# Optimization experiments

Measured on AMD Instinct MI355X. Metric: run time of the kernel, lower is better.

Reference implementation:

```python
import jax, jax.numpy as jnp
import numpy as np

NUM_GRAPHS = 2048
BN_EPS = 1e-5


def gcn_conv(x, W, b, src, dst, deg_isqrt):
    # PyG GCNConv: out = D^{-1/2} (A + I) D^{-1/2} X W + b
    h = x @ W  # [N, H]
    norm = deg_isqrt[src] * deg_isqrt[dst]  # [E]
    msg = h[src] * norm[:, None]            # [E, H]
    agg = jax.ops.segment_sum(msg, dst, num_segments=x.shape[0])
    agg = agg + h * (deg_isqrt * deg_isqrt)[:, None]  # self-loop term
    return agg + b


def batch_norm(x, gamma, beta):
    # training-mode BatchNorm1d over nodes (biased variance)
    mean = jnp.mean(x, axis=0)
    var = jnp.mean(jnp.square(x - mean), axis=0)
    return gamma * (x - mean) * jax.lax.rsqrt(var + BN_EPS) + beta


def pools(x, batch):
    ones = jnp.ones((x.shape[0],), x.dtype)
    cnt = jax.ops.segment_sum(ones, batch, num_segments=NUM_GRAPHS)  # [G]
    mean_p = jax.ops.segment_sum(x, batch, num_segments=NUM_GRAPHS) / jnp.maximum(cnt, 1.0)[:, None]
    max_p = jax.ops.segment_max(x, batch, num_segments=NUM_GRAPHS)
    max_p = jnp.where(cnt[:, None] > 0, max_p, 0.0)
    return jnp.concatenate([mean_p, max_p], axis=1)  # [G, 2H]


def setup_inputs() -> dict:
    key = jax.random.key(0)
    ks = jax.random.split(key, 32)
    N, E, D, H = 100000, 300000, 8, 256
    x = jax.random.normal(ks[0], (N, D), jnp.float32)
    edge_index = jax.random.randint(ks[1], (2, E), 0, N, jnp.int64)
    batch = jnp.sort(jax.random.randint(ks[2], (N,), 0, NUM_GRAPHS, jnp.int64))

    def lin(k, fi, fo):
        s = 1.0 / np.sqrt(fi)
        kw, kb = jax.random.split(k)
        return (jax.random.uniform(kw, (fi, fo), jnp.float32, -s, s),
                jax.random.uniform(kb, (fo,), jnp.float32, -s, s))

    W1, b1 = lin(ks[3], D, H)
    W2, b2 = lin(ks[4], H, H)
    W3, b3 = lin(ks[5], H, H)
    W4, b4 = lin(ks[6], H, H)
    g = jnp.ones((H,), jnp.float32)
    be = jnp.zeros((H,), jnp.float32)
    sW1, sb1 = lin(ks[7], 2 * H, 256)
    sW2, sb2 = lin(ks[8], 256, 128)
    hW1 = jnp.stack([lin(ks[9 + i], 128, 32)[0] for i in range(3)])
    hb1 = jnp.stack([lin(ks[9 + i], 128, 32)[1] for i in range(3)])
    hW2 = jnp.stack([lin(ks[12 + i], 32, 1)[0] for i in range(3)])
    hb2 = jnp.stack([lin(ks[12 + i], 32, 1)[1] for i in range(3)])
    return dict(x=x, edge_index=edge_index, batch=batch,
                W1=W1, b1=b1, W2=W2, b2=b2, W3=W3, b3=b3, W4=W4, b4=b4,
                g1=g, be1=be, g2=g, be2=be, g3=g, be3=be, g4=g, be4=be,
                sW1=sW1, sb1=sb1, sW2=sW2, sb2=sb2,
                hW1=hW1, hb1=hb1, hW2=hW2, hb2=hb2)


def reference(x, edge_index, batch, W1, b1, W2, b2, W3, b3, W4, b4,
              g1, be1, g2, be2, g3, be3, g4, be4,
              sW1, sb1, sW2, sb2, hW1, hb1, hW2, hb2):
    src, dst = edge_index[0], edge_index[1]
    N = x.shape[0]
    # degree with self-loops (GCN normalization)
    deg = jax.ops.segment_sum(jnp.ones((src.shape[0],), x.dtype), dst, num_segments=N) + 1.0
    deg_isqrt = jax.lax.rsqrt(deg)

    h = jax.nn.relu(batch_norm(gcn_conv(x, W1, b1, src, dst, deg_isqrt), g1, be1))
    h = jax.nn.relu(batch_norm(gcn_conv(h, W2, b2, src, dst, deg_isqrt), g2, be2))
    h = jax.nn.relu(batch_norm(gcn_conv(h, W3, b3, src, dst, deg_isqrt), g3, be3))
    h = jax.nn.relu(batch_norm(gcn_conv(h, W4, b4, src, dst, deg_isqrt), g4, be4))

    pooled = pools(h, batch)                               # [G, 512]
    s = jax.nn.relu(pooled @ sW1 + sb1)                    # dropout: eval -> identity
    s = jax.nn.relu(s @ sW2 + sb2)                         # [G, 128]
    # heads (vectorized over 3 tasks): [T, G]
    t = jax.nn.relu(jnp.einsum('gf,tfo->tgo', s, hW1) + hb1[:, None, :])
    out = (jnp.einsum('tgo,tof->tgf', t, hW2) + hb2[:, None, :])[..., 0]
    return out  # [num_tasks, G] == stacked list of squeezed head outputs
```

## Files before the change

### kernel.cpp

```cpp
#include <hip/hip_runtime.h>
#include <math.h>

#define TPB 256
#define NGRAPH 2048

typedef __attribute__((ext_vector_type(8))) short bf16x8;
typedef __attribute__((ext_vector_type(4))) float f32x4;

__device__ __forceinline__ unsigned short f2bf(float f) {
  unsigned u = __float_as_uint(f);
  unsigned r = (u + 0x7FFF + ((u >> 16) & 1)) >> 16;
  return (unsigned short)r;
}
__device__ __forceinline__ float bf2f(unsigned short h) {
  return __uint_as_float(((unsigned)h) << 16);
}

#define GLOAD_LDS16(G, L) \
  __builtin_amdgcn_global_load_lds((const __attribute__((address_space(1))) unsigned int*)(G), \
                                   (__attribute__((address_space(3))) unsigned int*)(L), 16, 0, 0)

__global__ void k_init(float* __restrict__ deg, int* __restrict__ cnt,
                       int* __restrict__ cntg, float* __restrict__ statsAll,
                       float* __restrict__ statsP, int N) {
  int i = blockIdx.x * TPB + threadIdx.x;
  if (i < N) { deg[i] = 1.0f; cnt[i] = 0; }
  if (i < NGRAPH) cntg[i] = 0;
  if (i < 2048) statsAll[i] = 0.f;
  if (i < 12288) statsP[i] = 0.f;
}

__global__ void k_deg_hist(const int* __restrict__ dst, float* __restrict__ deg,
                           int* __restrict__ cnt, int E) {
  int e = blockIdx.x * TPB + threadIdx.x;
  if (e < E) {
    int d = dst[e];
    atomicAdd(&deg[d], 1.0f);
    atomicAdd(&cnt[d], 1);
  }
}

__global__ void k_hist_batch(const int* __restrict__ batch, int* __restrict__ cntg, int N) {
  int i = blockIdx.x * TPB + threadIdx.x;
  if (i < N) atomicAdd(&cntg[batch[i]], 1);
}

__global__ void k_rsqrt(float* __restrict__ d, int N) {
  int i = blockIdx.x * TPB + threadIdx.x;
  if (i < N) d[i] = rsqrtf(d[i]);
}

__global__ void k_scan1(const int* __restrict__ in, int* __restrict__ out,
                        int* __restrict__ bsum, int n) {
  __shared__ int ts[256];
  int tid = threadIdx.x;
  int base = blockIdx.x * 1024 + tid * 4;
  int v0 = (base + 0 < n) ? in[base + 0] : 0;
  int v1 = (base + 1 < n) ? in[base + 1] : 0;
  int v2 = (base + 2 < n) ? in[base + 2] : 0;
  int v3 = (base + 3 < n) ? in[base + 3] : 0;
  int s = v0 + v1 + v2 + v3;
  int run = s;
  ts[tid] = run; __syncthreads();
  for (int off = 1; off < 256; off <<= 1) {
    int add = (tid >= off) ? ts[tid - off] : 0;
    __syncthreads();
    run += add; ts[tid] = run; __syncthreads();
  }
  int acc = run - s;
  if (base + 0 < n) out[base + 0] = acc; acc += v0;
  if (base + 1 < n) out[base + 1] = acc; acc += v1;
  if (base + 2 < n) out[base + 2] = acc; acc += v2;
  if (base + 3 < n) out[base + 3] = acc;
  if (tid == 255) bsum[blockIdx.x] = run;
}

__global__ void k_scan_small(const int* __restrict__ in, int* __restrict__ dst, int n) {
  __shared__ int ts[256];
  int tid = threadIdx.x;
  int chunk = (n + 255) >> 8;
  int start = tid * chunk;
  int s = 0;
  for (int j = 0; j < chunk; ++j) { int idx = start + j; if (idx < n) s += in[idx]; }
  int run = s;
  ts[tid] = run; __syncthreads();
  for (int off = 1; off < 256; off <<= 1) {
    int add = (tid >= off) ? ts[tid - off] : 0;
    __syncthreads();
    run += add; ts[tid] = run; __syncthreads();
  }
  int acc = run - s;
  for (int j = 0; j < chunk; ++j) {
    int idx = start + j;
    if (idx < n) { dst[idx] = acc; acc += in[idx]; }
  }
  if (tid == 255) dst[n] = run;
}

__global__ void k_scan3(int* __restrict__ rs, const int* __restrict__ bsumx,
                        int* __restrict__ cursor, int n, int total) {
  int i = blockIdx.x * TPB + threadIdx.x;
  if (i < n) {
    int v = rs[i] + bsumx[i >> 10];
    rs[i] = v; cursor[i] = v;
  }
  if (i == 0) rs[n] = total;
}

__global__ void k_scatter(const int* __restrict__ src, const int* __restrict__ dst,
                          int* __restrict__ cursor, int* __restrict__ es, int E) {
  int e = blockIdx.x * TPB + threadIdx.x;
  if (e < E) {
    int d = dst[e];
    int p = atomicAdd(&cursor[d], 1);
    es[p] = src[e];
  }
}

__global__ __launch_bounds__(256) void k_wprep2(const float* __restrict__ W,
    unsigned short* __restrict__ Wblk) {
  int c = blockIdx.x, k = threadIdx.x;
  float w = W[k * 256 + c];
  int t = k >> 6, kl = k & 63;
  Wblk[t * 16384 + c * 64 + (kl ^ ((c & 7) << 3))] = f2bf(w);
}

__global__ void k_agg8(const float* __restrict__ x, const float* __restrict__ dis,
                       const int* __restrict__ rs, const int* __restrict__ es,
                       float* __restrict__ xa8, int N) {
  int t = blockIdx.x * TPB + threadIdx.x;
  int n = t >> 3, c = t & 7;
  if (n >= N) return;
  int e0 = rs[n], e1 = rs[n + 1];
  float acc = 0.f;
  for (int e = e0; e < e1; ++e) {
    int s = es[e];
    acc += dis[s] * x[s * 8 + c];
  }
  float dn = dis[n];
  xa8[n * 8 + c] = dn * acc + dn * dn * x[n * 8 + c];
}

__global__ __launch_bounds__(256) void k_gemm8(const float* __restrict__ A,
    const float* __restrict__ W, const float* __restrict__ b,
    unsigned short* __restrict__ Ybf, float* __restrict__ stats, int N) {
  __shared__ float Ws[8 * 256];
  __shared__ float bs[256];
  __shared__ float rows[64 * 8];
  int tid = threadIdx.x;
  int row0 = blockIdx.x * 64;
  for (int j = 0; j < 8; ++j) Ws[tid + j * 256] = W[tid + j * 256];
  bs[tid] = b[tid];
  int lim = N * 8;
  int o0 = row0 * 8 + tid, o1 = o0 + 256;
  rows[tid] = (o0 < lim) ? A[o0] : 0.f;
  rows[tid + 256] = (o1 < lim) ? A[o1] : 0.f;
  __syncthreads();
  float s = 0.f, s2 = 0.f;
  for (int r = 0; r < 64; ++r) {
    int row = row0 + r;
    if (row >= N) break;
    float acc = bs[tid];
#pragma unroll
    for (int k = 0; k < 8; ++k) acc += rows[r * 8 + k] * Ws[k * 256 + tid];
    Ybf[(size_t)row * 256 + tid] = f2bf(acc);
    s += acc; s2 += acc * acc;
  }
  atomicAdd(&stats[tid], s);
  atomicAdd(&stats[256 + tid], s2);
}

__global__ __launch_bounds__(256) void k_agg_bn(const unsigned short* __restrict__ Ybf,
    const float* __restrict__ ss, const float* __restrict__ dis,
    const int* __restrict__ rs, const int* __restrict__ es,
    unsigned short* __restrict__ Ahi, int N) {
  int lane = threadIdx.x & 63;
  int n = __builtin_amdgcn_readfirstlane(blockIdx.x * 4 + (threadIdx.x >> 6));
  if (n >= N) return;
  int c = lane * 4;
  float4 sc = *(const float4*)&ss[c];
  float4 sh = *(const float4*)&ss[256 + c];
  int e0 = rs[n], e1 = rs[n + 1];
  float4 a = make_float4(0.f, 0.f, 0.f, 0.f);
  int e = e0;
  for (; e + 2 <= e1; e += 2) {
    int s0 = es[e], s1 = es[e + 1];
    float d0 = dis[s0], d1 = dis[s1];
    ushort4 y0 = *(const ushort4*)&Ybf[(size_t)s0 * 256 + c];
    ushort4 y1 = *(const ushort4*)&Ybf[(size_t)s1 * 256 + c];
    a.x += d0 * fmaxf(fmaf(bf2f(y0.x), sc.x, sh.x), 0.f)
         + d1 * fmaxf(fmaf(bf2f(y1.x), sc.x, sh.x), 0.f);
    a.y += d0 * fmaxf(fmaf(bf2f(y0.y), sc.y, sh.y), 0.f)
         + d1 * fmaxf(fmaf(bf2f(y1.y), sc.y, sh.y), 0.f);
    a.z += d0 * fmaxf(fmaf(bf2f(y0.z), sc.z, sh.z), 0.f)
         + d1 * fmaxf(fmaf(bf2f(y1.z), sc.z, sh.z), 0.f);
    a.w += d0 * fmaxf(fmaf(bf2f(y0.w), sc.w, sh.w), 0.f)
         + d1 * fmaxf(fmaf(bf2f(y1.w), sc.w, sh.w), 0.f);
  }
  if (e < e1) {
    int s0 = es[e];
    float d0 = dis[s0];
    ushort4 y0 = *(const ushort4*)&Ybf[(size_t)s0 * 256 + c];
    a.x += d0 * fmaxf(fmaf(bf2f(y0.x), sc.x, sh.x), 0.f);
    a.y += d0 * fmaxf(fmaf(bf2f(y0.y), sc.y, sh.y), 0.f);
    a.z += d0 * fmaxf(fmaf(bf2f(y0.z), sc.z, sh.z), 0.f);
    a.w += d0 * fmaxf(fmaf(bf2f(y0.w), sc.w, sh.w), 0.f);
  }
  float dn = dis[n];
  float dn2 = dn * dn;
  ushort4 yb = *(const ushort4*)&Ybf[(size_t)n * 256 + c];
  float4 r;
  r.x = dn * a.x + dn2 * fmaxf(fmaf(bf2f(yb.x), sc.x, sh.x), 0.f);
  r.y = dn * a.y + dn2 * fmaxf(fmaf(bf2f(yb.y), sc.y, sh.y), 0.f);
  r.z = dn * a.z + dn2 * fmaxf(fmaf(bf2f(yb.z), sc.z, sh.z), 0.f);
  r.w = dn * a.w + dn2 * fmaxf(fmaf(bf2f(yb.w), sc.w, sh.w), 0.f);
  ushort4 h;
  h.x = f2bf(r.x); h.y = f2bf(r.y); h.z = f2bf(r.z); h.w = f2bf(r.w);
  *(ushort4*)&Ahi[(size_t)n * 256 + c] = h;
}

__global__ __launch_bounds__(256) void k_gemm_mfma(
    const unsigned short* __restrict__ A,
    const unsigned short* __restrict__ Wblk,
    const float* __restrict__ bias, unsigned short* __restrict__ Ybf,
    float* __restrict__ statsP, int M) {
  __shared__ unsigned short Wlds[2][16384];
  __shared__ float bstats[512];
  const int tid = threadIdx.x;
  const int lane = tid & 63;
  const int w = tid >> 6;
  const int l15 = lane & 15, lg = lane >> 4;
  const int r0 = blockIdx.x * 128 + w * 32;

  bstats[tid] = 0.f;
  bstats[tid + 256] = 0.f;

  const unsigned short* Ap0 = A + (size_t)(r0 + l15) * 256 + lg * 8;
  const unsigned short* Ap1 = Ap0 + 16 * 256;
  bf16x8 a0[8], a1[8];
#pragma unroll
  for (int kk = 0; kk < 8; ++kk) {
    a0[kk] = *(const bf16x8*)(Ap0 + kk * 32);
    a1[kk] = *(const bf16x8*)(Ap1 + kk * 32);
  }

#define WSTAGE(buf, t)                                                        \
  {                                                                           \
    _Pragma("unroll")                                                         \
    for (int it = 0; it < 8; ++it)                                            \
      GLOAD_LDS16(Wblk + (t) * 16384 + it * 2048 + tid * 8,                   \
                  &Wlds[buf][it * 2048 + tid * 8]);                           \
  }
  WSTAGE(0, 0);
  asm volatile("s_waitcnt vmcnt(0)" ::: "memory");
  __builtin_amdgcn_s_barrier();

  f32x4 acc[2][16] = {};
  int cur = 0;
#pragma unroll
  for (int t = 0; t < 4; ++t) {
    if (t < 3) WSTAGE(cur ^ 1, t + 1);
#pragma unroll
    for (int kk2 = 0; kk2 < 2; ++kk2) {
      int kg = t * 2 + kk2;
#pragma unroll
      for (int n = 0; n < 16; ++n) {
        int c = n * 16 + l15;
        bf16x8 b = *(const bf16x8*)&Wlds[cur][c * 64 +
                     ((kk2 * 32 + lg * 8) ^ ((l15 & 7) << 3))];
        acc[0][n] = __builtin_amdgcn_mfma_f32_16x16x32_bf16(a0[kg], b, acc[0][n], 0, 0, 0);
        acc[1][n] = __builtin_amdgcn_mfma_f32_16x16x32_bf16(a1[kg], b, acc[1][n], 0, 0, 0);
      }
    }
    asm volatile("s_waitcnt vmcnt(0) lgkmcnt(0)" ::: "memory");
    __builtin_amdgcn_s_barrier();
    cur ^= 1;
  }

  unsigned short* ws = ((unsigned short*)&Wlds[0][0]) + w * 8192;
#pragma unroll
  for (int n = 0; n < 16; ++n) {
    int col = n * 16 + l15;
    float bv = bias[col];
    float s = 0.f, s2 = 0.f;
#pragma unroll
    for (int half = 0; half < 2; ++half) {
      f32x4 v = acc[half][n];
#pragma unroll
      for (int j = 0; j < 4; ++j) {
        float val = v[j] + bv;
        int rl = half * 16 + lg * 4 + j;
        ws[rl * 256 + col] = f2bf(val);
        if (r0 + rl < M) { s += val; s2 += val * val; }
      }
    }
    s += __shfl_xor(s, 16);  s += __shfl_xor(s, 32);
    s2 += __shfl_xor(s2, 16); s2 += __shfl_xor(s2, 32);
    if (lg == 0) {
      atomicAdd(&bstats[col], s);
      atomicAdd(&bstats[256 + col], s2);
    }
  }

#pragma unroll
  for (int it = 0; it < 16; ++it) {
    int idx = it * 64 + lane;
    int rl = idx >> 5;
    int c16 = idx & 31;
    int grow = r0 + rl;
    if (grow < M)
      *(int4*)((char*)Ybf + (size_t)grow * 512 + c16 * 16) =
          *(const int4*)((const char*)ws + rl * 512 + c16 * 16);
  }

  __syncthreads();
  float* sp = statsP + (blockIdx.x & 7) * 512;
  atomicAdd(&sp[tid], bstats[tid]);
  atomicAdd(&sp[256 + tid], bstats[256 + tid]);
}

__global__ void k_scaleshift(const float* __restrict__ base, int npart,
                             const float* __restrict__ g,
                             const float* __restrict__ be, float* __restrict__ ss, int N) {
  int c = threadIdx.x;
  float s = 0.f, s2 = 0.f;
  for (int p = 0; p < npart; ++p) {
    s += base[p * 512 + c];
    s2 += base[p * 512 + 256 + c];
  }
  float inv = 1.0f / (float)N;
  float mean = s * inv;
  float var = s2 * inv - mean * mean;
  var = fmaxf(var, 0.f);
  float sc = g[c] * rsqrtf(var + 1e-5f);
  ss[c] = sc;
  ss[256 + c] = be[c] - mean * sc;
}

__global__ __launch_bounds__(256) void k_pool(const unsigned short* __restrict__ Ybf,
    const float* __restrict__ ss, const int* __restrict__ gstart,
    float* __restrict__ pooled) {
  int g = blockIdx.x, c = threadIdx.x;
  float sc = ss[c], sh = ss[256 + c];
  int n0 = gstart[g], n1 = gstart[g + 1];
  float s = 0.f, m = 0.f;
  for (int n = n0; n < n1; ++n) {
    float v = fmaxf(fmaf(bf2f(Ybf[(size_t)n * 256 + c]), sc, sh), 0.f);
    s += v; m = fmaxf(m, v);
  }
  float cnt = (float)(n1 - n0);
  pooled[g * 512 + c] = s / fmaxf(cnt, 1.0f);
  pooled[g * 512 + 256 + c] = m;
}

__global__ __launch_bounds__(256) void k_mlp1(const float* __restrict__ P,
    const float* __restrict__ W, const float* __restrict__ b, float* __restrict__ O) {
  __shared__ float Ps[8 * 512];
  int tid = threadIdx.x;
  int g0 = blockIdx.x * 8;
  for (int j = 0; j < 16; ++j) Ps[tid + j * 256] = P[g0 * 512 + tid + j * 256];
  __syncthreads();
  float acc[8];
  float bb = b[tid];
#pragma unroll
  for (int gi = 0; gi < 8; ++gi) acc[gi] = bb;
  for (int k = 0; k < 512; ++k) {
    float w = W[k * 256 + tid];
#pragma unroll
    for (int gi = 0; gi < 8; ++gi) acc[gi] += Ps[gi * 512 + k] * w;
  }
  for (int gi = 0; gi < 8; ++gi)
    O[(g0 + gi) * 256 + tid] = fmaxf(acc[gi], 0.f);
}

__global__ __launch_bounds__(128) void k_mlp2(const float* __restrict__ S,
    const float* __restrict__ W, const float* __restrict__ b, float* __restrict__ O) {
  __shared__ float Ss[16 * 256];
  int tid = threadIdx.x;
  int g0 = blockIdx.x * 16;
  for (int j = 0; j < 32; ++j) Ss[tid + j * 128] = S[g0 * 256 + tid + j * 128];
  __syncthreads();
  float acc[16];
  float bb = b[tid];
#pragma unroll
  for (int gi = 0; gi < 16; ++gi) acc[gi] = bb;
  for (int k = 0; k < 256; ++k) {
    float w = W[k * 128 + tid];
#pragma unroll
    for (int gi = 0; gi < 16; ++gi) acc[gi] += Ss[gi * 256 + k] * w;
  }
  for (int gi = 0; gi < 16; ++gi)
    O[(g0 + gi) * 128 + tid] = fmaxf(acc[gi], 0.f);
}

__global__ __launch_bounds__(128) void k_heads(const float* __restrict__ S,
    const float* __restrict__ hW1, const float* __restrict__ hb1,
    const float* __restrict__ hW2, const float* __restrict__ hb2,
    float* __restrict__ out) {
  __shared__ float ssm[128];
  __shared__ float t1[96];
  int g = blockIdx.x, tid = threadIdx.x;
  ssm[tid] = S[g * 128 + tid];
  __syncthreads();
  if (tid < 96) {
    int t = tid >> 5, o = tid & 31;
    float acc = hb1[t * 32 + o];
    for (int k = 0; k < 128; ++k) acc += ssm[k] * hW1[t * 4096 + k * 32 + o];
    t1[tid] = fmaxf(acc, 0.f);
  }
  __syncthreads();
  if (tid < 3) {
    float acc = hb2[tid];
    for (int o = 0; o < 32; ++o) acc += t1[tid * 32 + o] * hW2[tid * 32 + o];
    out[tid * NGRAPH + g] = acc;
  }
}

extern "C" void kernel_launch(void* const* d_in, const int* in_sizes, int n_in,
                              void* d_out, int out_size, void* d_ws, size_t ws_size,
                              hipStream_t stream) {
  const float* x   = (const float*)d_in[0];
  const int* ei    = (const int*)d_in[1];
  const int* batch = (const int*)d_in[2];
  const float* W1 = (const float*)d_in[3];  const float* b1 = (const float*)d_in[4];
  const float* W2 = (const float*)d_in[5];  const float* b2 = (const float*)d_in[6];
  const float* W3 = (const float*)d_in[7];  const float* b3 = (const float*)d_in[8];
  const float* W4 = (const float*)d_in[9];  const float* b4 = (const float*)d_in[10];
  const float* g1 = (const float*)d_in[11]; const float* be1 = (const float*)d_in[12];
  const float* g2 = (const float*)d_in[13]; const float* be2 = (const float*)d_in[14];
  const float* g3 = (const float*)d_in[15]; const float* be3 = (const float*)d_in[16];
  const float* g4 = (const float*)d_in[17]; const float* be4 = (const float*)d_in[18];
  const float* sW1 = (const float*)d_in[19]; const float* sb1 = (const float*)d_in[20];
  const float* sW2 = (const float*)d_in[21]; const float* sb2 = (const float*)d_in[22];
  const float* hW1 = (const float*)d_in[23]; const float* hb1 = (const float*)d_in[24];
  const float* hW2 = (const float*)d_in[25]; const float* hb2 = (const float*)d_in[26];

  const int N = in_sizes[0] / 8;
  const int E = in_sizes[1] / 2;
  const int Npad = (N + 127) & ~127;
  const int* srcp = ei;
  const int* dstp = ei + E;

  char* base = (char*)d_ws;
  size_t off = 0;
  auto alloc = [&](size_t bytes) -> void* {
    void* p = base + off;
    off += (bytes + 255) & ~(size_t)255;
    return p;
  };
  unsigned short* Ybf = (unsigned short*)alloc((size_t)Npad * 256 * 2);
  unsigned short* Ahi = (unsigned short*)alloc((size_t)Npad * 256 * 2);
  float* dis  = (float*)alloc((size_t)N * 4);
  int* cnt    = (int*)alloc((size_t)N * 4);
  int* rs     = (int*)alloc((size_t)(N + 1) * 4);
  int* cursor = (int*)alloc((size_t)N * 4);
  int* es     = (int*)alloc((size_t)E * 4);
  int* bsum   = (int*)alloc(1024 * 4);
  int* bsumx  = (int*)alloc(1032 * 4);
  float* xa8  = (float*)alloc((size_t)N * 8 * 4);
  float* statsAll = (float*)alloc(2048 * 4);
  float* statsP   = (float*)alloc(12288 * 4);
  float* ssAll    = (float*)alloc(2048 * 4);
  unsigned short* Wblk = (unsigned short*)alloc(3 * 256 * 256 * 2);
  int* cntg    = (int*)alloc(2048 * 4);
  int* gstart  = (int*)alloc(2049 * 4);
  float* pooled = (float*)alloc((size_t)2048 * 512 * 4);
  float* s1b    = (float*)alloc((size_t)2048 * 256 * 4);
  float* s2b    = (float*)alloc((size_t)2048 * 128 * 4);
  (void)ws_size; (void)n_in; (void)out_size;

  int nb = (N + TPB - 1) / TPB;
  int eb = (E + TPB - 1) / TPB;
  int nblocks1 = (N + 1023) / 1024;

  k_init<<<nb, TPB, 0, stream>>>(dis, cnt, cntg, statsAll, statsP, N);
  k_deg_hist<<<eb, TPB, 0, stream>>>(dstp, dis, cnt, E);
  k_hist_batch<<<nb, TPB, 0, stream>>>(batch, cntg, N);
  k_rsqrt<<<nb, TPB, 0, stream>>>(dis, N);
  k_scan1<<<nblocks1, 256, 0, stream>>>(cnt, rs, bsum, N);
  k_scan_small<<<1, 256, 0, stream>>>(bsum, bsumx, nblocks1);
  k_scan3<<<nb, TPB, 0, stream>>>(rs, bsumx, cursor, N, E);
  k_scatter<<<eb, TPB, 0, stream>>>(srcp, dstp, cursor, es, E);
  k_scan_small<<<1, 256, 0, stream>>>(cntg, gstart, NGRAPH);

  k_wprep2<<<256, 256, 0, stream>>>(W2, Wblk + 0 * 65536);
  k_wprep2<<<256, 256, 0, stream>>>(W3, Wblk + 1 * 65536);
  k_wprep2<<<256, 256, 0, stream>>>(W4, Wblk + 2 * 65536);

  k_agg8<<<(N * 8 + TPB - 1) / TPB, TPB, 0, stream>>>(x, dis, rs, es, xa8, N);
  k_gemm8<<<(N + 63) / 64, 256, 0, stream>>>(xa8, W1, b1, Ybf, statsAll, N);
  k_scaleshift<<<1, 256, 0, stream>>>(statsAll, 1, g1, be1, ssAll, N);

  const float* bs_[3] = {b2, b3, b4};
  const float* gs[3]  = {g2, g3, g4};
  const float* bes[3] = {be2, be3, be4};
  for (int L = 0; L < 3; ++L) {
    k_agg_bn<<<(N + 3) / 4, 256, 0, stream>>>(Ybf, ssAll + L * 512, dis, rs, es,
                                              Ahi, N);
    k_gemm_mfma<<<Npad / 128, 256, 0, stream>>>(Ahi, Wblk + L * 65536,
                                                bs_[L], Ybf, statsP + L * 4096, N);
    k_scaleshift<<<1, 256, 0, stream>>>(statsP + L * 4096, 8, gs[L], bes[L],
                                        ssAll + (L + 1) * 512, N);
  }

  k_pool<<<NGRAPH, 256, 0, stream>>>(Ybf, ssAll + 3 * 512, gstart, pooled);
  k_mlp1<<<NGRAPH / 8, 256, 0, stream>>>(pooled, sW1, sb1, s1b);
  k_mlp2<<<NGRAPH / 16, 128, 0, stream>>>(s1b, sW2, sb2, s2b);
  k_heads<<<NGRAPH, 128, 0, stream>>>(s2b, hW1, hb1, hW2, hb2, (float*)d_out);
}
```

Baseline: 580.5 us.

## Halve GEMM row tile to 64 and single-buffer weight LDS staging

The MFMA GEMM now gives each block 64 rows instead of 128, with one 16-row tile per wave. Weights sit in a single 32KB LDS buffer instead of a double buffer, and A fragments are loaded per K-stage rather than all up front. This cuts LDS and register use per block and doubles the grid, which aims at higher occupancy and more parallelism across CUs. The costs are twice the total weight traffic from L2 and no overlap between the weight load and the MFMA work within a block.

Result: faster. 527.8 us (-9.1%).

```diff
diff --git a/kernel.cpp b/kernel.cpp
--- a/kernel.cpp
+++ b/kernel.cpp
@@ -224,75 +224,58 @@
     const unsigned short* __restrict__ Wblk,
     const float* __restrict__ bias, unsigned short* __restrict__ Ybf,
     float* __restrict__ statsP, int M) {
-  __shared__ unsigned short Wlds[2][16384];
+  __shared__ unsigned short Wlds[16384];
   __shared__ float bstats[512];
   const int tid = threadIdx.x;
   const int lane = tid & 63;
   const int w = tid >> 6;
   const int l15 = lane & 15, lg = lane >> 4;
-  const int r0 = blockIdx.x * 128 + w * 32;
+  const int r0 = blockIdx.x * 64 + w * 16;
 
   bstats[tid] = 0.f;
   bstats[tid + 256] = 0.f;
 
-  const unsigned short* Ap0 = A + (size_t)(r0 + l15) * 256 + lg * 8;
-  const unsigned short* Ap1 = Ap0 + 16 * 256;
-  bf16x8 a0[8], a1[8];
-#pragma unroll
-  for (int kk = 0; kk < 8; ++kk) {
-    a0[kk] = *(const bf16x8*)(Ap0 + kk * 32);
-    a1[kk] = *(const bf16x8*)(Ap1 + kk * 32);
-  }
-
-#define WSTAGE(buf, t)                                                        \
-  {                                                                           \
-    _Pragma("unroll")                                                         \
-    for (int it = 0; it < 8; ++it)                                            \
-      GLOAD_LDS16(Wblk + (t) * 16384 + it * 2048 + tid * 8,                   \
-                  &Wlds[buf][it * 2048 + tid * 8]);                           \
-  }
-  WSTAGE(0, 0);
-  asm volatile("s_waitcnt vmcnt(0)" ::: "memory");
-  __builtin_amdgcn_s_barrier();
-
-  f32x4 acc[2][16] = {};
-  int cur = 0;
+  const unsigned short* Ap = A + (size_t)(r0 + l15) * 256 + lg * 8;
+
+  f32x4 acc[16] = {};
 #pragma unroll
   for (int t = 0; t < 4; ++t) {
-    if (t < 3) WSTAGE(cur ^ 1, t + 1);
+#pragma unroll
+    for (int it = 0; it < 8; ++it)
+      GLOAD_LDS16(Wblk + t * 16384 + it * 2048 + tid * 8,
+                  &Wlds[it * 2048 + tid * 8]);
+    bf16x8 a0 = *(const bf16x8*)(Ap + t * 64);
+    bf16x8 a1 = *(const bf16x8*)(Ap + t * 64 + 32);
+    asm volatile("s_waitcnt vmcnt(0)" ::: "memory");
+    __builtin_amdgcn_s_barrier();
 #pragma unroll
     for (int kk2 = 0; kk2 < 2; ++kk2) {
-      int kg = t * 2 + kk2;
+      bf16x8 a = kk2 ? a1 : a0;
 #pragma unroll
       for (int n = 0; n < 16; ++n) {
         int c = n * 16 + l15;
-        bf16x8 b = *(const bf16x8*)&Wlds[cur][c * 64 +
+        bf16x8 b = *(const bf16x8*)&Wlds[c * 64 +
                      ((kk2 * 32 + lg * 8) ^ ((l15 & 7) << 3))];
-        acc[0][n] = __builtin_amdgcn_mfma_f32_16x16x32_bf16(a0[kg], b, acc[0][n], 0, 0, 0);
-        acc[1][n] = __builtin_amdgcn_mfma_f32_16x16x32_bf16(a1[kg], b, acc[1][n], 0, 0, 0);
+        acc[n] = __builtin_amdgcn_mfma_f32_16x16x32_bf16(a, b, acc[n], 0, 0, 0);
       }
     }
-    asm volatile("s_waitcnt vmcnt(0) lgkmcnt(0)" ::: "memory");
+    asm volatile("s_waitcnt lgkmcnt(0)" ::: "memory");
     __builtin_amdgcn_s_barrier();
-    cur ^= 1;
-  }
-
-  unsigned short* ws = ((unsigned short*)&Wlds[0][0]) + w * 8192;
+  }
+
+  unsigned short* stage = Wlds;
 #pragma unroll
   for (int n = 0; n < 16; ++n) {
     int col = n * 16 + l15;
     float bv = bias[col];
     float s = 0.f, s2 = 0.f;
-#pragma unroll
-    for (int half = 0; half < 2; ++half) {
-      f32x4 v = acc[half][n];
-#pragma unroll
-      for (int j = 0; j < 4; ++j) {
-        float val = v[j] + bv;
-        int rl = half * 16 + lg * 4 + j;
-        ws[rl * 256 + col] = f2bf(val);
-        if (r0 + rl < M) { s += val; s2 += val * val; }
-      }
+    f32x4 v = acc[n];
+#pragma unroll
+    for (int j = 0; j < 4; ++j) {
+      float val = v[j] + bv;
+      int rl = w * 16 + lg * 4 + j;
+      stage[rl * 256 + col] = f2bf(val);
+      if (blockIdx.x * 64 + rl < M) { s += val; s2 += val * val; }
     }
     s += __shfl_xor(s, 16);  s += __shfl_xor(s, 32);
     s2 += __shfl_xor(s2, 16); s2 += __shfl_xor(s2, 32);
@@ -301,19 +284,17 @@
       atomicAdd(&bstats[256 + col], s2);
     }
   }
-
-#pragma unroll
-  for (int it = 0; it < 16; ++it) {
-    int idx = it * 64 + lane;
+  __syncthreads();
+#pragma unroll
+  for (int it = 0; it < 8; ++it) {
+    int idx = it * 256 + tid;
     int rl = idx >> 5;
     int c16 = idx & 31;
-    int grow = r0 + rl;
+    int grow = blockIdx.x * 64 + rl;
     if (grow < M)
       *(int4*)((char*)Ybf + (size_t)grow * 512 + c16 * 16) =
-          *(const int4*)((const char*)ws + rl * 512 + c16 * 16);
-  }
-
-  __syncthreads();
+          *(const int4*)((const char*)stage + rl * 512 + c16 * 16);
+  }
   float* sp = statsP + (blockIdx.x & 7) * 512;
   atomicAdd(&sp[tid], bstats[tid]);
   atomicAdd(&sp[256 + tid], bstats[256 + tid]);
@@ -497,8 +478,8 @@
   for (int L = 0; L < 3; ++L) {
     k_agg_bn<<<(N + 3) / 4, 256, 0, stream>>>(Ybf, ssAll + L * 512, dis, rs, es,
                                               Ahi, N);
-    k_gemm_mfma<<<Npad / 128, 256, 0, stream>>>(Ahi, Wblk + L * 65536,
-                                                bs_[L], Ybf, statsP + L * 4096, N);
+    k_gemm_mfma<<<(N + 63) / 64, 256, 0, stream>>>(Ahi, Wblk + L * 65536,
+                                                   bs_[L], Ybf, statsP + L * 4096, N);
     k_scaleshift<<<1, 256, 0, stream>>>(statsP + L * 4096, 8, gs[L], bes[L],
                                         ssAll + (L + 1) * 512, N);
   }
```
